# Kernel tuning notes

Hardware: AMD Instinct MI355X
Metric: run time of the kernel (lower is better)

## Reference

```python
import jax, jax.numpy as jnp
import numpy as np
from jax import lax


def _conv1x1(x, w, b=None):
    # x: [N,C,H,W], w: [O,C]
    y = jnp.einsum('nchw,oc->nohw', x, w)
    if b is not None:
        y = y + b[None, :, None, None]
    return y


def _bn(x, g, b, rm, rv):
    # eval-mode BatchNorm2d, eps=1e-5 (torch default)
    inv = g / jnp.sqrt(rv + 1e-5)
    return x * inv[None, :, None, None] + (b - rm * inv)[None, :, None, None]


def setup_inputs() -> dict:
    key = jax.random.key(0)
    ks = jax.random.split(key, 32)
    N, C1, C2, H, W = 16, 256, 256, 64, 64
    mid = C2 // 16  # local_att reduction=16
    f32 = jnp.float32
    def nrm(k, shp, s=0.05):
        return s * jax.random.normal(k, shp, f32)
    return dict(
        x1=jax.random.normal(ks[0], (N, C1, H, W), f32),
        x2=jax.random.normal(ks[1], (N, C2, H, W), f32),
        conv1_w=nrm(ks[2], (C2, C1)), conv1_b=nrm(ks[3], (C2,)),
        conv2_w=nrm(ks[4], (C2, C2)), conv2_b=nrm(ks[5], (C2,)),
        conv3_w=nrm(ks[6], (C2, C2)), conv3_b=nrm(ks[7], (C2,)),
        conv4_w=nrm(ks[8], (C2, C2)), conv4_b=nrm(ks[9], (C2,)),
        conv4g_w=nrm(ks[10], (1, C2)), conv4g_b=nrm(ks[11], (1,)),
        bn_g=1.0 + nrm(ks[12], (C2,)), bn_b=nrm(ks[13], (C2,)),
        bn_rm=nrm(ks[14], (C2,)), bn_rv=1.0 + 0.1 * jax.random.uniform(ks[15], (C2,), f32),
        gamma=jax.random.normal(ks[16], (C2, 1, 1), f32), beta=jnp.zeros((C2, 1, 1), f32),
        gate_w=nrm(ks[17], (C2, C2)), gate_b=nrm(ks[18], (C2,)),
        dw_w=nrm(ks[19], (C2, 1, 3, 3)), dw_b=nrm(ks[20], (C2,)),
        interact_w=nrm(ks[21], (C2 // 4, C2 // 4)), interact_b=0.5 + nrm(ks[22], (C2 // 4,)),
        ca_w=nrm(ks[23], (1, 1, 5)),  # channel_att conv1d kernel, k=5 for C=256
        la1_w=nrm(ks[24], (mid, C2)),
        la_bn_g=1.0 + nrm(ks[25], (mid,)), la_bn_b=nrm(ks[26], (mid,)),
        la_bn_rm=nrm(ks[27], (mid,)), la_bn_rv=1.0 + 0.1 * jax.random.uniform(ks[28], (mid,), f32),
        fh_w=nrm(ks[29], (C2, mid)), fw_w=nrm(ks[30], (C2, mid)),
    )


def reference(x1, x2, conv1_w, conv1_b, conv2_w, conv2_b, conv3_w, conv3_b,
              conv4_w, conv4_b, conv4g_w, conv4g_b, bn_g, bn_b, bn_rm, bn_rv,
              gamma, beta, gate_w, gate_b, dw_w, dw_b, interact_w, interact_b,
              ca_w, la1_w, la_bn_g, la_bn_b, la_bn_rm, la_bn_rv, fh_w, fw_w):
    N, _, H, W = x1.shape
    C = conv1_w.shape[0]
    g1 = _conv1x1(x1, conv1_w, conv1_b)
    w1 = jax.nn.sigmoid(_bn(g1, bn_g, bn_b, bn_rm, bn_rv))
    g2 = _conv1x1(x2, conv2_w, conv2_b)
    w2 = jax.nn.sigmoid(_bn(g2, bn_g, bn_b, bn_rm, bn_rv))
    XG = g1 + g2

    # channel_att: GAP -> conv1d(k=5) across channels -> sigmoid gate
    y = XG.mean((2, 3))[:, None, :]  # [N,1,C]
    y = lax.conv_general_dilated(y, ca_w, (1,), [(2, 2)],
                                 dimension_numbers=('NCH', 'OIH', 'NCH'))
    temp = XG * jax.nn.sigmoid(y[:, 0, :])[:, :, None, None]

    # spatial sigmoid gate then 4-way group interact + softmax reweight
    Xs = jax.nn.sigmoid(_conv1x1(XG, conv4g_w, conv4g_b)) * XG
    C4 = C // 4
    Xr = Xs.reshape(N, 4, C4, H, W)
    o1 = jnp.einsum('ngchw,oc->ngohw', Xr, interact_w) + interact_b[None, None, :, None, None]
    xmap = o1.reshape(N, 4, 1, C4 * H * W)
    xav = xmap / xmap.mean(-1, keepdims=True)
    soft = jax.nn.softmax(xav, axis=2)  # softmax over size-1 dim -> ones (faithful)
    out = (soft.reshape(N, 4, C4, H, W) * Xr).reshape(N, C, H, W)

    # per-group (16) normalization using X_GOBAL stats (std unbiased, ddof=1)
    GN = 16
    xs = XG.reshape(N, GN, -1)
    mu = xs.mean(-1, keepdims=True)
    sd = jnp.std(xs, axis=-1, keepdims=True, ddof=1)
    x_gui = ((out.reshape(N, GN, -1) - mu) / (sd + 1e-10)).reshape(N, C, H, W)
    x_gui = x_gui * gamma[None] + beta[None]

    # threshold masks vs global-avg sigmoid reweights
    rw = jax.nn.sigmoid(XG.mean((2, 3), keepdims=True))  # [N,C,1,1]
    up1 = rw >= w1
    up2 = rw >= w2
    zero = jnp.zeros((), XG.dtype)
    x_up = jnp.where(up1, XG, zero) + jnp.where(up2, XG, zero)
    x_low = jnp.where(~up1, XG, zero) + jnp.where(~up2, XG, zero)

    # low branch: dwconv3x3 -> 1x1 -> channel-softmax gate
    dw = lax.conv_general_dilated(x_low, dw_w, (1, 1), [(1, 1), (1, 1)],
                                  dimension_numbers=('NCHW', 'OIHW', 'NCHW'),
                                  feature_group_count=C) + dw_b[None, :, None, None]
    x11 = _conv1x1(dw, conv3_w, conv3_b)
    gate = jax.nn.softmax(jax.nn.relu(x_low.mean((2, 3)) @ gate_w.T + gate_b), axis=1)
    xL = x11 * gate[:, :, None, None] + _conv1x1(x_up, conv4_w, conv4_b) + x_gui + temp

    # local_att (coordinate attention)
    xh = jnp.swapaxes(xL.mean(3, keepdims=True), 2, 3)  # [N,C,1,H]
    xw = xL.mean(2, keepdims=True)                       # [N,C,1,W]
    yc = jax.nn.relu(_bn(_conv1x1(jnp.concatenate([xh, xw], 3), la1_w),
                         la_bn_g, la_bn_b, la_bn_rm, la_bn_rv))
    sh = jax.nn.sigmoid(_conv1x1(jnp.swapaxes(yc[..., :H], 2, 3), fh_w))  # [N,C,H,1]
    sw = jax.nn.sigmoid(_conv1x1(yc[..., H:], fw_w))                      # [N,C,1,W]
    return xL * sh * sw
```

## Files before the change

### kernel.cpp

```cpp
#include <hip/hip_runtime.h>
#include <cstddef>
#include <cstdint>

constexpr int NN = 16, CC = 256, HH = 64, WW = 64, HW = 64 * 64;
constexpr size_t FSZ = (size_t)NN * CC * HW;

typedef short bf16x8 __attribute__((ext_vector_type(8)));
typedef float f32x4 __attribute__((ext_vector_type(4)));

__device__ __forceinline__ float sigmoidf_(float x) { return 1.f / (1.f + expf(-x)); }

__device__ __forceinline__ unsigned short bf16_rne(float f) {
    uint32_t u = __builtin_bit_cast(uint32_t, f);
    u += 0x7FFFu + ((u >> 16) & 1u);
    return (unsigned short)(u >> 16);
}
__device__ __forceinline__ float bf16_tof(unsigned short h) {
    uint32_t u = ((uint32_t)h) << 16;
    return __builtin_bit_cast(float, u);
}

__global__ __launch_bounds__(256) void wsplit_kernel(
    const float* __restrict__ w1, const float* __restrict__ w2,
    const float* __restrict__ w3, const float* __restrict__ w4,
    unsigned short* __restrict__ w1h, unsigned short* __restrict__ w1m, unsigned short* __restrict__ w1l,
    unsigned short* __restrict__ w2h, unsigned short* __restrict__ w2m, unsigned short* __restrict__ w2l,
    unsigned short* __restrict__ w4h, unsigned short* __restrict__ w4l,
    unsigned short* __restrict__ w3b,
    float* __restrict__ zstat, float* __restrict__ zspix) {
    const int i = blockIdx.x * 256 + threadIdx.x;
    {
        float x = w1[i];
        unsigned short h = bf16_rne(x); float r = x - bf16_tof(h);
        unsigned short m = bf16_rne(r); float r2 = r - bf16_tof(m);
        w1h[i] = h; w1m[i] = m; w1l[i] = bf16_rne(r2);
    }
    {
        float x = w2[i];
        unsigned short h = bf16_rne(x); float r = x - bf16_tof(h);
        unsigned short m = bf16_rne(r); float r2 = r - bf16_tof(m);
        w2h[i] = h; w2m[i] = m; w2l[i] = bf16_rne(r2);
    }
    {
        float x = w4[i];
        unsigned short h = bf16_rne(x); float r = x - bf16_tof(h);
        w4h[i] = h; w4l[i] = bf16_rne(r);
    }
    w3b[i] = bf16_rne(w3[i]);
    if (i < 8192) zstat[i] = 0.f;
    zspix[i] = 0.f;
}

template <int NS>
__global__ __launch_bounds__(256) void tsplit_kernel(const float* __restrict__ X,
                                                     unsigned short* __restrict__ O0,
                                                     unsigned short* __restrict__ O1,
                                                     unsigned short* __restrict__ O2) {
    const int hw0 = blockIdx.x * 64, c0 = blockIdx.y * 64, n = blockIdx.z;
    __shared__ float sT[64][65];
    const int tid = threadIdx.x;
    {
        const int hwl = (tid & 15) << 2;
        const int cl = tid >> 4;
#pragma unroll
        for (int p = 0; p < 4; ++p) {
            const int c = cl + p * 16;
            const float4 v = *(const float4*)(X + ((size_t)(n * CC + c0 + c)) * HW + hw0 + hwl);
            sT[c][hwl] = v.x; sT[c][hwl + 1] = v.y; sT[c][hwl + 2] = v.z; sT[c][hwl + 3] = v.w;
        }
    }
    __syncthreads();
    const int hwl = tid >> 2, cb = (tid & 3) << 4;
    unsigned short h[16], m[16], l[16];
#pragma unroll
    for (int j = 0; j < 16; ++j) {
        const float x = sT[cb + j][hwl];
        const unsigned short hh = bf16_rne(x);
        h[j] = hh;
        if (NS >= 2) {
            const float r = x - bf16_tof(hh);
            const unsigned short mm = bf16_rne(r);
            m[j] = mm;
            if (NS >= 3) l[j] = bf16_rne(r - bf16_tof(mm));
        }
    }
    const size_t ob = ((size_t)(n * HW + hw0 + hwl)) * 256 + c0 + cb;
    *(int4*)(O0 + ob) = *(int4*)&h[0]; *(int4*)(O0 + ob + 8) = *(int4*)&h[8];
    if (NS >= 2) { *(int4*)(O1 + ob) = *(int4*)&m[0]; *(int4*)(O1 + ob + 8) = *(int4*)&m[8]; }
    if (NS >= 3) { *(int4*)(O2 + ob) = *(int4*)&l[0]; *(int4*)(O2 + ob + 8) = *(int4*)&l[8]; }
}

template <int NS>
__device__ __forceinline__ void mfma_core2(const unsigned short* X0,
                                           const unsigned short* X1,
                                           const unsigned short* X2,
                                           const unsigned short* W0,
                                           const unsigned short* W1,
                                           const unsigned short* W2,
                                           int n, int hw0, int o0, f32x4 (&acc)[2][4]) {
    __shared__ unsigned short sX[NS][64][40];
    __shared__ unsigned short sW[NS][128][40];
    const int tid = threadIdx.x;
    const int lane = tid & 63, wv = tid >> 6, quad = lane >> 4, nlo = lane & 15;
    const int srow = tid >> 2, skoff = (tid & 3) << 3;
    const unsigned short* Xs[3] = {X0, X1, X2};
    const unsigned short* Ws[3] = {W0, W1, W2};
    const size_t xg = ((size_t)(n * HW + hw0 + srow)) * 256 + skoff;
    const size_t wg = ((size_t)(o0 + srow)) * 256 + skoff;
    for (int k0 = 0; k0 < 256; k0 += 32) {
#pragma unroll
        for (int s = 0; s < NS; ++s) {
            *(int4*)&sX[s][srow][skoff] = *(const int4*)(Xs[s] + xg + k0);
            *(int4*)&sW[s][srow][skoff] = *(const int4*)(Ws[s] + wg + k0);
            *(int4*)&sW[s][64 + srow][skoff] = *(const int4*)(Ws[s] + wg + 64 * 256 + k0);
        }
        __syncthreads();
        bf16x8 af[NS][2];
#pragma unroll
        for (int s = 0; s < NS; ++s) {
            af[s][0] = *(const bf16x8*)&sW[s][wv * 16 + nlo][quad * 8];
            af[s][1] = *(const bf16x8*)&sW[s][64 + wv * 16 + nlo][quad * 8];
        }
#pragma unroll
        for (int nt = 0; nt < 4; ++nt) {
            bf16x8 bfr[NS];
#pragma unroll
            for (int s = 0; s < NS; ++s) bfr[s] = *(const bf16x8*)&sX[s][nt * 16 + nlo][quad * 8];
#pragma unroll
            for (int f = 0; f < 2; ++f) {
                if (NS == 3) {
                    acc[f][nt] = __builtin_amdgcn_mfma_f32_16x16x32_bf16(af[1][f], bfr[1], acc[f][nt], 0, 0, 0);
                    acc[f][nt] = __builtin_amdgcn_mfma_f32_16x16x32_bf16(af[0][f], bfr[2], acc[f][nt], 0, 0, 0);
                    acc[f][nt] = __builtin_amdgcn_mfma_f32_16x16x32_bf16(af[2][f], bfr[0], acc[f][nt], 0, 0, 0);
                    acc[f][nt] = __builtin_amdgcn_mfma_f32_16x16x32_bf16(af[0][f], bfr[1], acc[f][nt], 0, 0, 0);
                    acc[f][nt] = __builtin_amdgcn_mfma_f32_16x16x32_bf16(af[1][f], bfr[0], acc[f][nt], 0, 0, 0);
                    acc[f][nt] = __builtin_amdgcn_mfma_f32_16x16x32_bf16(af[0][f], bfr[0], acc[f][nt], 0, 0, 0);
                } else if (NS == 2) {
                    acc[f][nt] = __builtin_amdgcn_mfma_f32_16x16x32_bf16(af[0][f], bfr[1], acc[f][nt], 0, 0, 0);
                    acc[f][nt] = __builtin_amdgcn_mfma_f32_16x16x32_bf16(af[1][f], bfr[0], acc[f][nt], 0, 0, 0);
                    acc[f][nt] = __builtin_amdgcn_mfma_f32_16x16x32_bf16(af[0][f], bfr[0], acc[f][nt], 0, 0, 0);
                } else {
                    acc[f][nt] = __builtin_amdgcn_mfma_f32_16x16x32_bf16(af[0][f], bfr[0], acc[f][nt], 0, 0, 0);
                }
            }
        }
        __syncthreads();
    }
}

template <int NS>
__global__ __launch_bounds__(256, 3) void gemm_mfma_kernel(
    const unsigned short* __restrict__ X0, const unsigned short* __restrict__ X1,
    const unsigned short* __restrict__ X2, const unsigned short* __restrict__ W0,
    const unsigned short* __restrict__ W1, const unsigned short* __restrict__ W2,
    const float* __restrict__ bias, float* __restrict__ Y) {
    const int hw0 = blockIdx.x * 64, o0 = blockIdx.y * 128, n = blockIdx.z;
    f32x4 acc[2][4] = {};
    mfma_core2<NS>(X0, X1, X2, W0, W1, W2, n, hw0, o0, acc);
    const int lane = threadIdx.x & 63, wv = threadIdx.x >> 6;
    const int quad = lane >> 4, nlo = lane & 15;
#pragma unroll
    for (int f = 0; f < 2; ++f) {
        const int om = o0 + f * 64 + wv * 16 + quad * 4;
#pragma unroll
        for (int nt = 0; nt < 4; ++nt) {
            const int hw = hw0 + nt * 16 + nlo;
#pragma unroll
            for (int r = 0; r < 4; ++r) {
                const int o = om + r;
                Y[((size_t)(n * CC + o)) * HW + hw] = acc[f][nt][r] + bias[o];
            }
        }
    }
}

__global__ __launch_bounds__(256, 3) void gemm_xg_kernel(
    const unsigned short* __restrict__ X0, const unsigned short* __restrict__ X1,
    const unsigned short* __restrict__ X2, const unsigned short* __restrict__ W0,
    const unsigned short* __restrict__ W1, const unsigned short* __restrict__ W2,
    const float* __restrict__ bias, const float* __restrict__ g1,
    const float* __restrict__ cgw,
    float* __restrict__ XG, float* __restrict__ sum_c, float* __restrict__ sq_c,
    float* __restrict__ s_pix) {
    const int hw0 = blockIdx.x * 64, o0 = blockIdx.y * 128, n = blockIdx.z;
    f32x4 acc[2][4] = {};
    mfma_core2<3>(X0, X1, X2, W0, W1, W2, n, hw0, o0, acc);
    __shared__ float sRed[4][64];
    const int lane = threadIdx.x & 63, wv = threadIdx.x >> 6;
    const int quad = lane >> 4, nlo = lane & 15;
    float pnt[4] = {0.f, 0.f, 0.f, 0.f};
#pragma unroll
    for (int f = 0; f < 2; ++f) {
        const int om = o0 + f * 64 + wv * 16 + quad * 4;
#pragma unroll
        for (int r = 0; r < 4; ++r) {
            const int o = om + r;
            const float b = bias[o];
            const float wg = cgw[o];
            float s = 0.f, q = 0.f;
#pragma unroll
            for (int nt = 0; nt < 4; ++nt) {
                const int hw = hw0 + nt * 16 + nlo;
                const size_t rowi = ((size_t)(n * CC + o)) * HW + hw;
                const float xg = acc[f][nt][r] + b + g1[rowi];
                XG[rowi] = xg;
                s += xg; q += xg * xg;
                pnt[nt] += wg * xg;
            }
#pragma unroll
            for (int off = 1; off < 16; off <<= 1) { s += __shfl_xor(s, off); q += __shfl_xor(q, off); }
            if (nlo == 0) { atomicAdd(&sum_c[n * CC + o], s); atomicAdd(&sq_c[n * CC + o], q); }
        }
    }
#pragma unroll
    for (int nt = 0; nt < 4; ++nt) {
        float p = pnt[nt];
        p += __shfl_xor(p, 16); p += __shfl_xor(p, 32);
        if (quad == 0) sRed[wv][nt * 16 + nlo] = p;
    }
    __syncthreads();
    if (threadIdx.x < 64) {
        const float s2 = sRed[0][threadIdx.x] + sRed[1][threadIdx.x] +
                         sRed[2][threadIdx.x] + sRed[3][threadIdx.x];
        atomicAdd(&s_pix[n * HW + hw0 + threadIdx.x], s2);
    }
}

__global__ __launch_bounds__(256, 3) void gemm_final_kernel(
    const unsigned short* __restrict__ X0, const unsigned short* __restrict__ W0,
    const float* __restrict__ bias,
    const float* __restrict__ A, const float* __restrict__ XG, const float* __restrict__ s_pix,
    const float* __restrict__ cgb,
    const float* __restrict__ gate, const float* __restrict__ ca_sig,
    const float* __restrict__ mu_g, const float* __restrict__ isd_g,
    const float* __restrict__ gamma, const float* __restrict__ beta,
    float* __restrict__ out) {
    const int hw0 = blockIdx.x * 64, o0 = blockIdx.y * 128, n = blockIdx.z;
    f32x4 acc[2][4] = {};
    mfma_core2<1>(X0, nullptr, nullptr, W0, nullptr, nullptr, n, hw0, o0, acc);
    const int lane = threadIdx.x & 63, wv = threadIdx.x >> 6;
    const int quad = lane >> 4, nlo = lane & 15;
    const float cgb0 = cgb[0];
#pragma unroll
    for (int f = 0; f < 2; ++f) {
        const int om = o0 + f * 64 + wv * 16 + quad * 4;
#pragma unroll
        for (int nt = 0; nt < 4; ++nt) {
            const int hw = hw0 + nt * 16 + nlo;
            const int pix = n * HW + hw;
            const float sp = sigmoidf_(s_pix[pix] + cgb0);
#pragma unroll
            for (int r = 0; r < 4; ++r) {
                const int o = om + r;
                const float g = gate[n * CC + o];
                const float cs = ca_sig[n * CC + o];
                const float mu = mu_g[n * 16 + (o >> 4)];
                const float isd = isd_g[n * 16 + (o >> 4)];
                const size_t rowi = ((size_t)(n * CC + o)) * HW + hw;
                const float xg = XG[rowi];
                const float gui = (sp * xg - mu) * isd * gamma[o] + beta[o];
                out[rowi] = (acc[f][nt][r] + bias[o]) * g + A[rowi] + gui + xg * cs;
            }
        }
    }
}

__global__ __launch_bounds__(256) void stats2_kernel(const float* __restrict__ sum_c,
                                                     const float* __restrict__ sq_c,
                                                     const float* __restrict__ caw,
                                                     float* __restrict__ rw,
                                                     float* __restrict__ ca_sig,
                                                     float* __restrict__ mu_g,
                                                     float* __restrict__ isd_g,
                                                     float* __restrict__ xlow_sum) {
    const int n = blockIdx.x, c = threadIdx.x;
    __shared__ float m[256];
    const float mean = sum_c[n * CC + c] * (1.f / (float)HW);
    m[c] = mean;
    rw[n * CC + c] = sigmoidf_(mean);
    xlow_sum[n * CC + c] = 0.f;
    __syncthreads();
    float y = 0.f;
#pragma unroll
    for (int k = 0; k < 5; ++k) {
        const int cc = c - 2 + k;
        if (cc >= 0 && cc < 256) y += m[cc] * caw[k];
    }
    ca_sig[n * CC + c] = sigmoidf_(y);
    if (c < 16) {
        float S = 0.f, Q = 0.f;
        for (int j = 0; j < 16; ++j) {
            S += sum_c[n * CC + c * 16 + j];
            Q += sq_c[n * CC + c * 16 + j];
        }
        const float cnt = 65536.f;
        const float mu = S / cnt;
        float var = (Q - S * S / cnt) * (1.f / (cnt - 1.f));
        var = fmaxf(var, 0.f);
        mu_g[n * 16 + c] = mu;
        isd_g[n * 16 + c] = 1.f / (sqrtf(var) + 1e-10f);
    }
}

__global__ __launch_bounds__(256) void masks_split_kernel(
    float* g1_xlow,
    const float* __restrict__ XG,
    const float* __restrict__ rw,
    const float* __restrict__ bng, const float* __restrict__ bnb,
    const float* __restrict__ bnrm, const float* __restrict__ bnrv,
    unsigned short* __restrict__ O0, unsigned short* __restrict__ O1,
    float* __restrict__ xlow_sum) {
    const int hw0 = blockIdx.x * 64, c0 = blockIdx.y * 64, n = blockIdx.z;
    __shared__ float sT[64][65];
    const int tid = threadIdx.x;
    const int cl = tid >> 2;
    const int q = tid & 3;
    const int c = c0 + cl;
    const float inv = bng[c] / sqrtf(bnrv[c] + 1e-5f);
    const float off = bnb[c] - bnrm[c] * inv;
    const float rwv = rw[n * CC + c];
    const size_t rowb = ((size_t)(n * CC + c)) * HW + hw0;
    float lsum = 0.f;
#pragma unroll
    for (int j = 0; j < 4; ++j) {
        const int hwl = q * 4 + j * 16;
        const float4 a = *(const float4*)(g1_xlow + rowb + hwl);
        const float4 x = *(const float4*)(XG + rowb + hwl);
        const float* ap = &a.x; const float* xp = &x.x;
        float4 xlv;
        float* xlp = &xlv.x;
#pragma unroll
        for (int e = 0; e < 4; ++e) {
            const float g2e = xp[e] - ap[e];
            const float w1 = sigmoidf_(inv * ap[e] + off);
            const float w2 = sigmoidf_(inv * g2e + off);
            const float cu = (rwv >= w1 ? 1.f : 0.f) + (rwv >= w2 ? 1.f : 0.f);
            const float xu = xp[e] * cu;
            const float xl = xp[e] * (2.f - cu);
            sT[cl][hwl + e] = xu;
            xlp[e] = xl;
            lsum += xl;
        }
        *(float4*)(g1_xlow + rowb + hwl) = xlv;
    }
    lsum += __shfl_xor(lsum, 1);
    lsum += __shfl_xor(lsum, 2);
    if (q == 0) atomicAdd(&xlow_sum[n * CC + c], lsum);
    __syncthreads();
    const int hwl2 = tid >> 2, cb = (tid & 3) << 4;
    unsigned short h[16], m[16];
#pragma unroll
    for (int j = 0; j < 16; ++j) {
        const float x = sT[cb + j][hwl2];
        const unsigned short hh = bf16_rne(x);
        h[j] = hh;
        m[j] = bf16_rne(x - bf16_tof(hh));
    }
    const size_t ob = ((size_t)(n * HW + hw0 + hwl2)) * 256 + c0 + cb;
    *(int4*)(O0 + ob) = *(int4*)&h[0]; *(int4*)(O0 + ob + 8) = *(int4*)&h[8];
    *(int4*)(O1 + ob) = *(int4*)&m[0]; *(int4*)(O1 + ob + 8) = *(int4*)&m[8];
}

__global__ __launch_bounds__(256) void gate_kernel(const float* __restrict__ xlow_sum,
                                                   const float* __restrict__ gatew,
                                                   const float* __restrict__ gateb,
                                                   float* __restrict__ gate) {
    const int n = blockIdx.x, c = threadIdx.x;
    __shared__ float xm[256];
    __shared__ float red[256];
    xm[c] = xlow_sum[n * CC + c] * (1.f / (float)HW);
    __syncthreads();
    float acc = gateb[c];
    const float* wr = gatew + (size_t)c * 256;
#pragma unroll 8
    for (int k = 0; k < 256; ++k) acc += xm[k] * wr[k];
    const float v = fmaxf(acc, 0.f);
    red[c] = v;
    __syncthreads();
    for (int s = 128; s > 0; s >>= 1) {
        if (c < s) red[c] = fmaxf(red[c], red[c + s]);
        __syncthreads();
    }
    const float mx = red[0];
    __syncthreads();
    const float e = expf(v - mx);
    red[c] = e;
    __syncthreads();
    for (int s = 128; s > 0; s >>= 1) {
        if (c < s) red[c] += red[c + s];
        __syncthreads();
    }
    gate[n * CC + c] = e / red[0];
}

__global__ __launch_bounds__(256) void dwconv_kernel(const float* __restrict__ xlow,
                                                     const float* __restrict__ dww,
                                                     const float* __restrict__ dwb,
                                                     float* __restrict__ out) {
    const int c = blockIdx.x & 255;
    __shared__ float sl[64][65];
    const size_t base = (size_t)blockIdx.x * HW;
    for (int r = 0; r < 16; ++r) {
        const int idx = threadIdx.x + r * 256;
        sl[idx >> 6][idx & 63] = xlow[base + idx];
    }
    float wk[9];
#pragma unroll
    for (int j = 0; j < 9; ++j) wk[j] = dww[c * 9 + j];
    const float bias = dwb[c];
    __syncthreads();
    for (int r = 0; r < 16; ++r) {
        const int idx = threadIdx.x + r * 256;
        const int h = idx >> 6, w = idx & 63;
        float acc = bias;
#pragma unroll
        for (int dh = 0; dh < 3; ++dh) {
            const int hh = h + dh - 1;
            if (hh < 0 || hh > 63) continue;
#pragma unroll
            for (int dw2 = 0; dw2 < 3; ++dw2) {
                const int ww2 = w + dw2 - 1;
                if (ww2 < 0 || ww2 > 63) continue;
                acc += sl[hh][ww2] * wk[dh * 3 + dw2];
            }
        }
        out[base + idx] = acc;
    }
}

__global__ __launch_bounds__(256) void pool_kernel(const float* __restrict__ xL,
                                                   float* __restrict__ xh,
                                                   float* __restrict__ xw) {
    __shared__ float sl[64][65];
    const size_t base = (size_t)blockIdx.x * HW;
    for (int r = 0; r < 16; ++r) {
        const int idx = threadIdx.x + r * 256;
        sl[idx >> 6][idx & 63] = xL[base + idx];
    }
    __syncthreads();
    const int t = threadIdx.x;
    if (t < 64) {
        float s = 0.f;
        for (int w = 0; w < 64; ++w) s += sl[t][w];
        xh[(size_t)blockIdx.x * 64 + t] = s * (1.f / 64.f);
    } else if (t < 128) {
        const int w = t - 64;
        float s = 0.f;
        for (int h = 0; h < 64; ++h) s += sl[h][w];
        xw[(size_t)blockIdx.x * 64 + w] = s * (1.f / 64.f);
    }
}

__global__ __launch_bounds__(256) void local_att_kernel(const float* __restrict__ xh,
                                                        const float* __restrict__ xw,
                                                        const float* __restrict__ la1w,
                                                        const float* __restrict__ lag,
                                                        const float* __restrict__ lab,
                                                        const float* __restrict__ larm,
                                                        const float* __restrict__ larv,
                                                        const float* __restrict__ fhw,
                                                        const float* __restrict__ fww,
                                                        float* __restrict__ sh,
                                                        float* __restrict__ sw) {
    const int n = blockIdx.x;
    __shared__ float w1s[16 * 256];
    __shared__ float fhs[256 * 16];
    __shared__ float fws[256 * 16];
    __shared__ float ycs[16][128];
    for (int i = threadIdx.x; i < 4096; i += 256) {
        w1s[i] = la1w[i];
        fhs[i] = fhw[i];
        fws[i] = fww[i];
    }
    __syncthreads();
    for (int idx = threadIdx.x; idx < 2048; idx += 256) {
        const int m = idx >> 7, p = idx & 127;
        const float* vsrc = (p < 64) ? (xh + (size_t)n * CC * 64 + p)
                                     : (xw + (size_t)n * CC * 64 + (p - 64));
        float acc = 0.f;
#pragma unroll 8
        for (int c = 0; c < 256; ++c) acc += w1s[m * 256 + c] * vsrc[(size_t)c * 64];
        const float inv = lag[m] / sqrtf(larv[m] + 1e-5f);
        const float off = lab[m] - larm[m] * inv;
        ycs[m][p] = fmaxf(inv * acc + off, 0.f);
    }
    __syncthreads();
    for (int idx = threadIdx.x; idx < 16384; idx += 256) {
        const int c = idx >> 6, h = idx & 63;
        float a1 = 0.f, a2 = 0.f;
#pragma unroll
        for (int m = 0; m < 16; ++m) {
            a1 += fhs[c * 16 + m] * ycs[m][h];
            a2 += fws[c * 16 + m] * ycs[m][64 + h];
        }
        sh[(size_t)n * CC * 64 + idx] = sigmoidf_(a1);
        sw[(size_t)n * CC * 64 + idx] = sigmoidf_(a2);
    }
}

__global__ __launch_bounds__(256) void final_kernel(float* __restrict__ out,
                                                    const float* __restrict__ sh,
                                                    const float* __restrict__ sw) {
    __shared__ float shs[64], sws[64];
    const int t = threadIdx.x;
    if (t < 64) shs[t] = sh[(size_t)blockIdx.x * 64 + t];
    else if (t < 128) sws[t - 64] = sw[(size_t)blockIdx.x * 64 + (t - 64)];
    __syncthreads();
    const size_t base = (size_t)blockIdx.x * HW;
#pragma unroll 4
    for (int r = 0; r < 16; ++r) {
        const int idx = t + r * 256;
        out[base + idx] *= shs[idx >> 6] * sws[idx & 63];
    }
}

extern "C" void kernel_launch(void* const* d_in, const int* in_sizes, int n_in,
                              void* d_out, int out_size, void* d_ws, size_t ws_size,
                              hipStream_t stream) {
    const float* x1 = (const float*)d_in[0];
    const float* x2 = (const float*)d_in[1];
    const float* c1w = (const float*)d_in[2];
    const float* c1b = (const float*)d_in[3];
    const float* c2w = (const float*)d_in[4];
    const float* c2b = (const float*)d_in[5];
    const float* c3w = (const float*)d_in[6];
    const float* c3b = (const float*)d_in[7];
    const float* c4w = (const float*)d_in[8];
    const float* c4b = (const float*)d_in[9];
    const float* cgw = (const float*)d_in[10];
    const float* cgb = (const float*)d_in[11];
    const float* bng = (const float*)d_in[12];
    const float* bnb = (const float*)d_in[13];
    const float* bnrm = (const float*)d_in[14];
    const float* bnrv = (const float*)d_in[15];
    const float* gamma = (const float*)d_in[16];
    const float* beta = (const float*)d_in[17];
    const float* gatew = (const float*)d_in[18];
    const float* gateb = (const float*)d_in[19];
    const float* dww = (const float*)d_in[20];
    const float* dwb = (const float*)d_in[21];
    const float* caw = (const float*)d_in[24];
    const float* la1w = (const float*)d_in[25];
    const float* lag = (const float*)d_in[26];
    const float* lab = (const float*)d_in[27];
    const float* larm = (const float*)d_in[28];
    const float* larv = (const float*)d_in[29];
    const float* fhw = (const float*)d_in[30];
    const float* fww = (const float*)d_in[31];

    float* ws = (float*)d_ws;
    float* buf0 = ws;
    float* buf1 = ws + FSZ;
    float* buf2 = ws + 2 * FSZ;
    float* sp = ws + 3 * FSZ;
    float* sum_c = sp;    sp += 4096;
    float* sq_c = sp;     sp += 4096;
    float* rw = sp;       sp += 4096;
    float* ca_sig = sp;   sp += 4096;
    float* xlow_sum = sp; sp += 4096;
    float* mu_g = sp;     sp += 256;
    float* isd_g = sp;    sp += 256;
    float* s_pix = sp;    sp += (size_t)NN * HW;
    float* xh = sp;       sp += (size_t)NN * CC * 64;
    float* xwb = sp;      sp += (size_t)NN * CC * 64;
    float* shb = sp;      sp += (size_t)NN * CC * 64;
    float* swb = sp;      sp += (size_t)NN * CC * 64;
    unsigned short* wsp = (unsigned short*)shb;
    unsigned short* w1h = wsp + 0 * 65536;
    unsigned short* w1m = wsp + 1 * 65536;
    unsigned short* w1l = wsp + 2 * 65536;
    unsigned short* w2h = wsp + 3 * 65536;
    unsigned short* w2m = wsp + 4 * 65536;
    unsigned short* w2l = wsp + 5 * 65536;
    unsigned short* w4h = wsp + 6 * 65536;
    unsigned short* w4l = wsp + 7 * 65536;
    unsigned short* w3b = wsp + 8 * 65536;

    float* out = (float*)d_out;

    const dim3 gt(HW / 64, CC / 64, NN);
    const dim3 gg(HW / 64, CC / 128, NN);

    wsplit_kernel<<<256, 256, 0, stream>>>(c1w, c2w, c3w, c4w, w1h, w1m, w1l,
                                           w2h, w2m, w2l, w4h, w4l, w3b,
                                           sum_c, s_pix);
    {
        unsigned short* sx0 = (unsigned short*)buf1;
        unsigned short* sx1 = (unsigned short*)buf1 + FSZ;
        unsigned short* sx2 = (unsigned short*)buf2;
        tsplit_kernel<3><<<gt, 256, 0, stream>>>(x1, sx0, sx1, sx2);
        gemm_mfma_kernel<3><<<gg, 256, 0, stream>>>(sx0, sx1, sx2, w1h, w1m, w1l, c1b, buf0);
    }
    {
        unsigned short* sx0 = (unsigned short*)out;
        unsigned short* sx1 = (unsigned short*)out + FSZ;
        unsigned short* sx2 = (unsigned short*)buf2;
        tsplit_kernel<3><<<gt, 256, 0, stream>>>(x2, sx0, sx1, sx2);
        gemm_xg_kernel<<<gg, 256, 0, stream>>>(sx0, sx1, sx2, w2h, w2m, w2l, c2b,
                                               buf0, cgw, buf1, sum_c, sq_c, s_pix);
    }
    stats2_kernel<<<NN, 256, 0, stream>>>(sum_c, sq_c, caw, rw, ca_sig, mu_g, isd_g, xlow_sum);
    {
        unsigned short* ux0 = (unsigned short*)out;
        unsigned short* ux1 = (unsigned short*)out + FSZ;
        masks_split_kernel<<<gt, 256, 0, stream>>>(buf0, buf1, rw, bng, bnb, bnrm, bnrv,
                                                   ux0, ux1, xlow_sum);
    }
    float* gate = sum_c;
    gate_kernel<<<NN, 256, 0, stream>>>(xlow_sum, gatew, gateb, gate);
    dwconv_kernel<<<NN * CC, 256, 0, stream>>>(buf0, dww, dwb, buf2);
    {
        unsigned short* sx0 = (unsigned short*)buf0;
        tsplit_kernel<1><<<gt, 256, 0, stream>>>(buf2, sx0, nullptr, nullptr);
    }
    {
        unsigned short* ux0 = (unsigned short*)out;
        unsigned short* ux1 = (unsigned short*)out + FSZ;
        gemm_mfma_kernel<2><<<gg, 256, 0, stream>>>(ux0, ux1, nullptr, w4h, w4l, nullptr,
                                                    c4b, buf2);
    }
    {
        unsigned short* sx0 = (unsigned short*)buf0;
        gemm_final_kernel<<<gg, 256, 0, stream>>>(sx0, w3b, c3b, buf2, buf1, s_pix, cgb,
                                                  gate, ca_sig, mu_g, isd_g, gamma, beta, out);
    }
    pool_kernel<<<NN * CC, 256, 0, stream>>>(out, xh, xwb);
    local_att_kernel<<<NN, 256, 0, stream>>>(xh, xwb, la1w, lag, lab, larm, larv,
                                             fhw, fww, shb, swb);
    final_kernel<<<NN * CC, 256, 0, stream>>>(out, shb, swb);
}
```

Measured before the change: 675.6 us.

## Pre-swizzle GEMM operands into MFMA fragment layout and drop LDS staging

Weights and activations are now written by the split kernels directly in a 16x32 MFMA-fragment-tiled order, so each lane can load its bf16x8 operand with one contiguous global load. The GEMM core no longer stages tiles through shared memory or synchronizes, and each block now computes all 256 output channels (4x4 fragments per wave) instead of 128. This is meant to remove LDS traffic and barriers. In exchange, every wave reads its operands straight from global/L2 with no reuse across waves, uses more accumulator registers, and launches half as many GEMM blocks.

New measurement: 898.9 us. 33.1% more time.

```diff
diff --git a/kernel.cpp b/kernel.cpp
--- a/kernel.cpp
+++ b/kernel.cpp
@@ -19,6 +19,7 @@
     uint32_t u = ((uint32_t)h) << 16;
     return __builtin_bit_cast(float, u);
 }
+
 
 __global__ __launch_bounds__(256) void wsplit_kernel(
     const float* __restrict__ w1, const float* __restrict__ w2,
@@ -29,24 +30,27 @@
     unsigned short* __restrict__ w3b,
     float* __restrict__ zstat, float* __restrict__ zspix) {
     const int i = blockIdx.x * 256 + threadIdx.x;
+    const int o = i >> 8, c = i & 255;
+    const size_t fo = ((size_t)((o >> 4) * 8 + (c >> 5))) * 512 +
+                      (size_t)(((c & 31) >> 3) * 128 + (o & 15) * 8 + (c & 7));
     {
         float x = w1[i];
         unsigned short h = bf16_rne(x); float r = x - bf16_tof(h);
         unsigned short m = bf16_rne(r); float r2 = r - bf16_tof(m);
-        w1h[i] = h; w1m[i] = m; w1l[i] = bf16_rne(r2);
+        w1h[fo] = h; w1m[fo] = m; w1l[fo] = bf16_rne(r2);
     }
     {
         float x = w2[i];
         unsigned short h = bf16_rne(x); float r = x - bf16_tof(h);
         unsigned short m = bf16_rne(r); float r2 = r - bf16_tof(m);
-        w2h[i] = h; w2m[i] = m; w2l[i] = bf16_rne(r2);
+        w2h[fo] = h; w2m[fo] = m; w2l[fo] = bf16_rne(r2);
     }
     {
         float x = w4[i];
         unsigned short h = bf16_rne(x); float r = x - bf16_tof(h);
-        w4h[i] = h; w4l[i] = bf16_rne(r);
-    }
-    w3b[i] = bf16_rne(w3[i]);
+        w4h[fo] = h; w4l[fo] = bf16_rne(r);
+    }
+    w3b[fo] = bf16_rne(w3[i]);
     if (i < 8192) zstat[i] = 0.f;
     zspix[i] = 0.f;
 }
@@ -70,64 +74,66 @@
         }
     }
     __syncthreads();
-    const int hwl = tid >> 2, cb = (tid & 3) << 4;
-    unsigned short h[16], m[16], l[16];
-#pragma unroll
-    for (int j = 0; j < 16; ++j) {
-        const float x = sT[cb + j][hwl];
-        const unsigned short hh = bf16_rne(x);
-        h[j] = hh;
-        if (NS >= 2) {
-            const float r = x - bf16_tof(hh);
-            const unsigned short mm = bf16_rne(r);
-            m[j] = mm;
-            if (NS >= 3) l[j] = bf16_rne(r - bf16_tof(mm));
-        }
-    }
-    const size_t ob = ((size_t)(n * HW + hw0 + hwl)) * 256 + c0 + cb;
-    *(int4*)(O0 + ob) = *(int4*)&h[0]; *(int4*)(O0 + ob + 8) = *(int4*)&h[8];
-    if (NS >= 2) { *(int4*)(O1 + ob) = *(int4*)&m[0]; *(int4*)(O1 + ob + 8) = *(int4*)&m[8]; }
-    if (NS >= 3) { *(int4*)(O2 + ob) = *(int4*)&l[0]; *(int4*)(O2 + ob + 8) = *(int4*)&l[8]; }
+    const int lane = tid & 63, g = tid >> 6;
+    const int quad = lane >> 4, nlo = lane & 15;
+    const int hwl = g * 16 + nlo;
+#pragma unroll
+    for (int cs = 0; cs < 2; ++cs) {
+        const int clb = cs * 32 + quad * 8;
+        unsigned short h[8], m[8], l[8];
+#pragma unroll
+        for (int j = 0; j < 8; ++j) {
+            const float x = sT[clb + j][hwl];
+            const unsigned short hh = bf16_rne(x);
+            h[j] = hh;
+            if (NS >= 2) {
+                const float r = x - bf16_tof(hh);
+                const unsigned short mm = bf16_rne(r);
+                m[j] = mm;
+                if (NS >= 3) l[j] = bf16_rne(r - bf16_tof(mm));
+            }
+        }
+        const size_t ob = ((size_t)((n * 256 + (hw0 >> 4) + g) * 8 + (c0 >> 5) + cs)) * 512 +
+                          (size_t)lane * 8;
+        *(int4*)(O0 + ob) = *(int4*)&h[0];
+        if (NS >= 2) *(int4*)(O1 + ob) = *(int4*)&m[0];
+        if (NS >= 3) *(int4*)(O2 + ob) = *(int4*)&l[0];
+    }
 }
 
 template <int NS>
-__device__ __forceinline__ void mfma_core2(const unsigned short* X0,
-                                           const unsigned short* X1,
-                                           const unsigned short* X2,
-                                           const unsigned short* W0,
-                                           const unsigned short* W1,
-                                           const unsigned short* W2,
-                                           int n, int hw0, int o0, f32x4 (&acc)[2][4]) {
-    __shared__ unsigned short sX[NS][64][40];
-    __shared__ unsigned short sW[NS][128][40];
+__device__ __forceinline__ void mfma_frag_core(const unsigned short* __restrict__ X0,
+                                               const unsigned short* __restrict__ X1,
+                                               const unsigned short* __restrict__ X2,
+                                               const unsigned short* __restrict__ W0,
+                                               const unsigned short* __restrict__ W1,
+                                               const unsigned short* __restrict__ W2,
+                                               int n, int hw0, f32x4 (&acc)[4][4]) {
     const int tid = threadIdx.x;
-    const int lane = tid & 63, wv = tid >> 6, quad = lane >> 4, nlo = lane & 15;
-    const int srow = tid >> 2, skoff = (tid & 3) << 3;
+    const int lane = tid & 63, wv = tid >> 6;
     const unsigned short* Xs[3] = {X0, X1, X2};
     const unsigned short* Ws[3] = {W0, W1, W2};
-    const size_t xg = ((size_t)(n * HW + hw0 + srow)) * 256 + skoff;
-    const size_t wg = ((size_t)(o0 + srow)) * 256 + skoff;
-    for (int k0 = 0; k0 < 256; k0 += 32) {
-#pragma unroll
-        for (int s = 0; s < NS; ++s) {
-            *(int4*)&sX[s][srow][skoff] = *(const int4*)(Xs[s] + xg + k0);
-            *(int4*)&sW[s][srow][skoff] = *(const int4*)(Ws[s] + wg + k0);
-            *(int4*)&sW[s][64 + srow][skoff] = *(const int4*)(Ws[s] + wg + 64 * 256 + k0);
-        }
-        __syncthreads();
-        bf16x8 af[NS][2];
-#pragma unroll
-        for (int s = 0; s < NS; ++s) {
-            af[s][0] = *(const bf16x8*)&sW[s][wv * 16 + nlo][quad * 8];
-            af[s][1] = *(const bf16x8*)&sW[s][64 + wv * 16 + nlo][quad * 8];
-        }
+    const unsigned short* xp[NS];
+    const unsigned short* wp[NS];
+#pragma unroll
+    for (int s = 0; s < NS; ++s) {
+        xp[s] = Xs[s] + ((size_t)(n * 256 + (hw0 >> 4)) * 8) * 512 + (size_t)lane * 8;
+        wp[s] = Ws[s] + ((size_t)(wv * 4) * 8) * 512 + (size_t)lane * 8;
+    }
+    for (int ks = 0; ks < 8; ++ks) {
+        bf16x8 af[NS][4];
+#pragma unroll
+        for (int s = 0; s < NS; ++s)
+#pragma unroll
+            for (int f = 0; f < 4; ++f)
+                af[s][f] = *(const bf16x8*)(wp[s] + f * (8 * 512));
 #pragma unroll
         for (int nt = 0; nt < 4; ++nt) {
             bf16x8 bfr[NS];
 #pragma unroll
-            for (int s = 0; s < NS; ++s) bfr[s] = *(const bf16x8*)&sX[s][nt * 16 + nlo][quad * 8];
-#pragma unroll
-            for (int f = 0; f < 2; ++f) {
+            for (int s = 0; s < NS; ++s) bfr[s] = *(const bf16x8*)(xp[s] + nt * (8 * 512));
+#pragma unroll
+            for (int f = 0; f < 4; ++f) {
                 if (NS == 3) {
                     acc[f][nt] = __builtin_amdgcn_mfma_f32_16x16x32_bf16(af[1][f], bfr[1], acc[f][nt], 0, 0, 0);
                     acc[f][nt] = __builtin_amdgcn_mfma_f32_16x16x32_bf16(af[0][f], bfr[2], acc[f][nt], 0, 0, 0);
@@ -144,7 +150,8 @@
                 }
             }
         }
-        __syncthreads();
+#pragma unroll
+        for (int s = 0; s < NS; ++s) { xp[s] += 512; wp[s] += 512; }
     }
 }
 
@@ -154,14 +161,14 @@
     const unsigned short* __restrict__ X2, const unsigned short* __restrict__ W0,
     const unsigned short* __restrict__ W1, const unsigned short* __restrict__ W2,
     const float* __restrict__ bias, float* __restrict__ Y) {
-    const int hw0 = blockIdx.x * 64, o0 = blockIdx.y * 128, n = blockIdx.z;
-    f32x4 acc[2][4] = {};
-    mfma_core2<NS>(X0, X1, X2, W0, W1, W2, n, hw0, o0, acc);
+    const int hw0 = blockIdx.x * 64, n = blockIdx.z;
+    f32x4 acc[4][4] = {};
+    mfma_frag_core<NS>(X0, X1, X2, W0, W1, W2, n, hw0, acc);
     const int lane = threadIdx.x & 63, wv = threadIdx.x >> 6;
     const int quad = lane >> 4, nlo = lane & 15;
 #pragma unroll
-    for (int f = 0; f < 2; ++f) {
-        const int om = o0 + f * 64 + wv * 16 + quad * 4;
+    for (int f = 0; f < 4; ++f) {
+        const int om = wv * 64 + f * 16 + quad * 4;
 #pragma unroll
         for (int nt = 0; nt < 4; ++nt) {
             const int hw = hw0 + nt * 16 + nlo;
@@ -182,16 +189,16 @@
     const float* __restrict__ cgw,
     float* __restrict__ XG, float* __restrict__ sum_c, float* __restrict__ sq_c,
     float* __restrict__ s_pix) {
-    const int hw0 = blockIdx.x * 64, o0 = blockIdx.y * 128, n = blockIdx.z;
-    f32x4 acc[2][4] = {};
-    mfma_core2<3>(X0, X1, X2, W0, W1, W2, n, hw0, o0, acc);
+    const int hw0 = blockIdx.x * 64, n = blockIdx.z;
+    f32x4 acc[4][4] = {};
+    mfma_frag_core<3>(X0, X1, X2, W0, W1, W2, n, hw0, acc);
     __shared__ float sRed[4][64];
     const int lane = threadIdx.x & 63, wv = threadIdx.x >> 6;
     const int quad = lane >> 4, nlo = lane & 15;
     float pnt[4] = {0.f, 0.f, 0.f, 0.f};
 #pragma unroll
-    for (int f = 0; f < 2; ++f) {
-        const int om = o0 + f * 64 + wv * 16 + quad * 4;
+    for (int f = 0; f < 4; ++f) {
+        const int om = wv * 64 + f * 16 + quad * 4;
 #pragma unroll
         for (int r = 0; r < 4; ++r) {
             const int o = om + r;
@@ -235,15 +242,15 @@
     const float* __restrict__ mu_g, const float* __restrict__ isd_g,
     const float* __restrict__ gamma, const float* __restrict__ beta,
     float* __restrict__ out) {
-    const int hw0 = blockIdx.x * 64, o0 = blockIdx.y * 128, n = blockIdx.z;
-    f32x4 acc[2][4] = {};
-    mfma_core2<1>(X0, nullptr, nullptr, W0, nullptr, nullptr, n, hw0, o0, acc);
+    const int hw0 = blockIdx.x * 64, n = blockIdx.z;
+    f32x4 acc[4][4] = {};
+    mfma_frag_core<1>(X0, nullptr, nullptr, W0, nullptr, nullptr, n, hw0, acc);
     const int lane = threadIdx.x & 63, wv = threadIdx.x >> 6;
     const int quad = lane >> 4, nlo = lane & 15;
     const float cgb0 = cgb[0];
 #pragma unroll
-    for (int f = 0; f < 2; ++f) {
-        const int om = o0 + f * 64 + wv * 16 + quad * 4;
+    for (int f = 0; f < 4; ++f) {
+        const int om = wv * 64 + f * 16 + quad * 4;
 #pragma unroll
         for (int nt = 0; nt < 4; ++nt) {
             const int hw = hw0 + nt * 16 + nlo;
@@ -347,18 +354,25 @@
     lsum += __shfl_xor(lsum, 2);
     if (q == 0) atomicAdd(&xlow_sum[n * CC + c], lsum);
     __syncthreads();
-    const int hwl2 = tid >> 2, cb = (tid & 3) << 4;
-    unsigned short h[16], m[16];
-#pragma unroll
-    for (int j = 0; j < 16; ++j) {
-        const float x = sT[cb + j][hwl2];
-        const unsigned short hh = bf16_rne(x);
-        h[j] = hh;
-        m[j] = bf16_rne(x - bf16_tof(hh));
-    }
-    const size_t ob = ((size_t)(n * HW + hw0 + hwl2)) * 256 + c0 + cb;
-    *(int4*)(O0 + ob) = *(int4*)&h[0]; *(int4*)(O0 + ob + 8) = *(int4*)&h[8];
-    *(int4*)(O1 + ob) = *(int4*)&m[0]; *(int4*)(O1 + ob + 8) = *(int4*)&m[8];
+    const int lane = tid & 63, g = tid >> 6;
+    const int quad2 = lane >> 4, nlo = lane & 15;
+    const int hwl2 = g * 16 + nlo;
+#pragma unroll
+    for (int cs = 0; cs < 2; ++cs) {
+        const int clb = cs * 32 + quad2 * 8;
+        unsigned short h[8], m[8];
+#pragma unroll
+        for (int j = 0; j < 8; ++j) {
+            const float x = sT[clb + j][hwl2];
+            const unsigned short hh = bf16_rne(x);
+            h[j] = hh;
+            m[j] = bf16_rne(x - bf16_tof(hh));
+        }
+        const size_t ob = ((size_t)((n * 256 + (hw0 >> 4) + g) * 8 + (c0 >> 5) + cs)) * 512 +
+                          (size_t)lane * 8;
+        *(int4*)(O0 + ob) = *(int4*)&h[0];
+        *(int4*)(O1 + ob) = *(int4*)&m[0];
+    }
 }
 
 __global__ __launch_bounds__(256) void gate_kernel(const float* __restrict__ xlow_sum,
@@ -579,7 +593,7 @@
     float* out = (float*)d_out;
 
     const dim3 gt(HW / 64, CC / 64, NN);
-    const dim3 gg(HW / 64, CC / 128, NN);
+    const dim3 gg(HW / 64, 1, NN);
 
     wsplit_kernel<<<256, 256, 0, stream>>>(c1w, c2w, c3w, c4w, w1h, w1m, w1l,
                                            w2h, w2m, w2l, w4h, w4l, w3b,
```

## Pre-swizzle weights into MFMA fragment layout and double-buffer activation tiles

Applied to the files above, without the earlier changes.

Weights are now written in an MFMA-fragment-ordered layout during the split pass, so each wave loads its A fragments directly from global memory instead of staging them through shared memory. Activation tiles are double-buffered in LDS: the next k-slice is fetched into registers while the current one is consumed by MFMAs, which cuts one barrier per iteration and lets loads overlap compute. This lowers LDS footprint and traffic. The cost is more global weight loads per block, relying on L2/cache reuse across blocks, and higher register pressure from the prefetch.

After: 653.0 us. 3.3% less time.

```diff
diff --git a/kernel.cpp b/kernel.cpp
--- a/kernel.cpp
+++ b/kernel.cpp
@@ -19,6 +19,7 @@
     uint32_t u = ((uint32_t)h) << 16;
     return __builtin_bit_cast(float, u);
 }
+
 
 __global__ __launch_bounds__(256) void wsplit_kernel(
     const float* __restrict__ w1, const float* __restrict__ w2,
@@ -29,24 +30,27 @@
     unsigned short* __restrict__ w3b,
     float* __restrict__ zstat, float* __restrict__ zspix) {
     const int i = blockIdx.x * 256 + threadIdx.x;
+    const int o = i >> 8, c = i & 255;
+    const size_t fo = ((size_t)((o >> 4) * 8 + (c >> 5))) * 512 +
+                      (size_t)(((c & 31) >> 3) * 128 + (o & 15) * 8 + (c & 7));
     {
         float x = w1[i];
         unsigned short h = bf16_rne(x); float r = x - bf16_tof(h);
         unsigned short m = bf16_rne(r); float r2 = r - bf16_tof(m);
-        w1h[i] = h; w1m[i] = m; w1l[i] = bf16_rne(r2);
+        w1h[fo] = h; w1m[fo] = m; w1l[fo] = bf16_rne(r2);
     }
     {
         float x = w2[i];
         unsigned short h = bf16_rne(x); float r = x - bf16_tof(h);
         unsigned short m = bf16_rne(r); float r2 = r - bf16_tof(m);
-        w2h[i] = h; w2m[i] = m; w2l[i] = bf16_rne(r2);
+        w2h[fo] = h; w2m[fo] = m; w2l[fo] = bf16_rne(r2);
     }
     {
         float x = w4[i];
         unsigned short h = bf16_rne(x); float r = x - bf16_tof(h);
-        w4h[i] = h; w4l[i] = bf16_rne(r);
-    }
-    w3b[i] = bf16_rne(w3[i]);
+        w4h[fo] = h; w4l[fo] = bf16_rne(r);
+    }
+    w3b[fo] = bf16_rne(w3[i]);
     if (i < 8192) zstat[i] = 0.f;
     zspix[i] = 0.f;
 }
@@ -91,41 +95,48 @@
 }
 
 template <int NS>
-__device__ __forceinline__ void mfma_core2(const unsigned short* X0,
-                                           const unsigned short* X1,
-                                           const unsigned short* X2,
-                                           const unsigned short* W0,
-                                           const unsigned short* W1,
-                                           const unsigned short* W2,
+__device__ __forceinline__ void mfma_core4(const unsigned short* __restrict__ X0,
+                                           const unsigned short* __restrict__ X1,
+                                           const unsigned short* __restrict__ X2,
+                                           const unsigned short* __restrict__ W0,
+                                           const unsigned short* __restrict__ W1,
+                                           const unsigned short* __restrict__ W2,
                                            int n, int hw0, int o0, f32x4 (&acc)[2][4]) {
-    __shared__ unsigned short sX[NS][64][40];
-    __shared__ unsigned short sW[NS][128][40];
+    __shared__ unsigned short sX[2][NS][64][40];
     const int tid = threadIdx.x;
     const int lane = tid & 63, wv = tid >> 6, quad = lane >> 4, nlo = lane & 15;
     const int srow = tid >> 2, skoff = (tid & 3) << 3;
     const unsigned short* Xs[3] = {X0, X1, X2};
     const unsigned short* Ws[3] = {W0, W1, W2};
     const size_t xg = ((size_t)(n * HW + hw0 + srow)) * 256 + skoff;
-    const size_t wg = ((size_t)(o0 + srow)) * 256 + skoff;
-    for (int k0 = 0; k0 < 256; k0 += 32) {
-#pragma unroll
-        for (int s = 0; s < NS; ++s) {
-            *(int4*)&sX[s][srow][skoff] = *(const int4*)(Xs[s] + xg + k0);
-            *(int4*)&sW[s][srow][skoff] = *(const int4*)(Ws[s] + wg + k0);
-            *(int4*)&sW[s][64 + srow][skoff] = *(const int4*)(Ws[s] + wg + 64 * 256 + k0);
-        }
-        __syncthreads();
+    const unsigned short* wp[NS];
+#pragma unroll
+    for (int s = 0; s < NS; ++s)
+        wp[s] = Ws[s] + ((size_t)((o0 >> 4) + wv) * 8) * 512 + (size_t)lane * 8;
+
+#pragma unroll
+    for (int s = 0; s < NS; ++s)
+        *(int4*)&sX[0][s][srow][skoff] = *(const int4*)(Xs[s] + xg);
+    __syncthreads();
+
+    for (int ks = 0; ks < 8; ++ks) {
+        const int cur = ks & 1;
+        int4 nx[NS];
+        if (ks < 7) {
+#pragma unroll
+            for (int s = 0; s < NS; ++s) nx[s] = *(const int4*)(Xs[s] + xg + (ks + 1) * 32);
+        }
         bf16x8 af[NS][2];
 #pragma unroll
-        for (int s = 0; s < NS; ++s) {
-            af[s][0] = *(const bf16x8*)&sW[s][wv * 16 + nlo][quad * 8];
-            af[s][1] = *(const bf16x8*)&sW[s][64 + wv * 16 + nlo][quad * 8];
-        }
+        for (int s = 0; s < NS; ++s)
+#pragma unroll
+            for (int f = 0; f < 2; ++f)
+                af[s][f] = *(const bf16x8*)(wp[s] + ((size_t)(f * 32 + ks)) * 512);
 #pragma unroll
         for (int nt = 0; nt < 4; ++nt) {
             bf16x8 bfr[NS];
 #pragma unroll
-            for (int s = 0; s < NS; ++s) bfr[s] = *(const bf16x8*)&sX[s][nt * 16 + nlo][quad * 8];
+            for (int s = 0; s < NS; ++s) bfr[s] = *(const bf16x8*)&sX[cur][s][nt * 16 + nlo][quad * 8];
 #pragma unroll
             for (int f = 0; f < 2; ++f) {
                 if (NS == 3) {
@@ -144,6 +155,10 @@
                 }
             }
         }
+        if (ks < 7) {
+#pragma unroll
+            for (int s = 0; s < NS; ++s) *(int4*)&sX[cur ^ 1][s][srow][skoff] = nx[s];
+        }
         __syncthreads();
     }
 }
@@ -156,7 +171,7 @@
     const float* __restrict__ bias, float* __restrict__ Y) {
     const int hw0 = blockIdx.x * 64, o0 = blockIdx.y * 128, n = blockIdx.z;
     f32x4 acc[2][4] = {};
-    mfma_core2<NS>(X0, X1, X2, W0, W1, W2, n, hw0, o0, acc);
+    mfma_core4<NS>(X0, X1, X2, W0, W1, W2, n, hw0, o0, acc);
     const int lane = threadIdx.x & 63, wv = threadIdx.x >> 6;
     const int quad = lane >> 4, nlo = lane & 15;
 #pragma unroll
@@ -184,7 +199,7 @@
     float* __restrict__ s_pix) {
     const int hw0 = blockIdx.x * 64, o0 = blockIdx.y * 128, n = blockIdx.z;
     f32x4 acc[2][4] = {};
-    mfma_core2<3>(X0, X1, X2, W0, W1, W2, n, hw0, o0, acc);
+    mfma_core4<3>(X0, X1, X2, W0, W1, W2, n, hw0, o0, acc);
     __shared__ float sRed[4][64];
     const int lane = threadIdx.x & 63, wv = threadIdx.x >> 6;
     const int quad = lane >> 4, nlo = lane & 15;
@@ -237,7 +252,7 @@
     float* __restrict__ out) {
     const int hw0 = blockIdx.x * 64, o0 = blockIdx.y * 128, n = blockIdx.z;
     f32x4 acc[2][4] = {};
-    mfma_core2<1>(X0, nullptr, nullptr, W0, nullptr, nullptr, n, hw0, o0, acc);
+    mfma_core4<1>(X0, nullptr, nullptr, W0, nullptr, nullptr, n, hw0, o0, acc);
     const int lane = threadIdx.x & 63, wv = threadIdx.x >> 6;
     const int quad = lane >> 4, nlo = lane & 15;
     const float cgb0 = cgb[0];
```
